# Kernel optimization log

Measured on AMD Instinct MI355X. Metric: run time of the kernel, lower is better.

Reference implementation:

```python
import jax, jax.numpy as jnp
import numpy as np
from jax.ops import segment_sum


def gcn_conv(x, src, dst, W, b, num_nodes):
    # PyG GCNConv: x' = D^{-1/2} (A + I) D^{-1/2} (x @ W) + b
    loops = jnp.arange(num_nodes, dtype=src.dtype)
    s = jnp.concatenate([src, loops])  # source of each edge (incl. self-loops)
    d = jnp.concatenate([dst, loops])  # destination of each edge
    ones = jnp.ones(s.shape[0], dtype=x.dtype)
    deg = segment_sum(ones, d, num_segments=num_nodes)  # in-degree incl. self-loop
    dinv = jnp.where(deg > 0, jax.lax.rsqrt(deg), 0.0)
    norm = dinv[s] * dinv[d]  # [E+N]
    h = x @ W  # [N, C_out] dense transform first (C_out <= C_in typical)
    msg = h[s] * norm[:, None]  # gather + scale  [E+N, C_out]
    out = segment_sum(msg, d, num_segments=num_nodes)  # scatter-add
    return out + b


def setup_inputs() -> dict:
    key = jax.random.key(0)
    k1, k2, k3, k4 = jax.random.split(key, 4)
    N, E = 100000, 1600000
    C_in, C_out = 64, 32
    C_hid = 2 * C_out
    x = jax.random.normal(k1, (N, C_in), dtype=jnp.float32)
    edge_index = jax.random.randint(k2, (2, E), 0, N, dtype=jnp.int64)
    # Glorot-style init for the linear weights, zero bias (PyG defaults)
    W1 = jax.random.normal(k3, (C_in, C_hid), dtype=jnp.float32) * (1.0 / np.sqrt(C_in))
    b1 = jnp.zeros((C_hid,), dtype=jnp.float32)
    W2 = jax.random.normal(k4, (C_hid, C_out), dtype=jnp.float32) * (1.0 / np.sqrt(C_hid))
    b2 = jnp.zeros((C_out,), dtype=jnp.float32)
    return {"x": x, "edge_index": edge_index, "num_nodes": N,
            "W1": W1, "b1": b1, "W2": W2, "b2": b2}


def reference(x, edge_index, num_nodes, W1, b1, W2, b2):
    src, dst = edge_index[0], edge_index[1]
    h = gcn_conv(x, src, dst, W1, b1, num_nodes)
    h = jax.nn.relu(h)
    out = gcn_conv(h, src, dst, W2, b2, num_nodes)
    return out
```

## Files before the change

kernel.cpp:

```cpp
#include <hip/hip_runtime.h>


constexpr int CAP = 4096;
constexpr int NBMAX = 1024;
constexpr int SBCAP = 40960;
constexpr int NSBMAX = 64;
constexpr float QS = 2048.f;
constexpr float QSI = 1.f / 2048.f;

__device__ inline int sxlo(unsigned u) { return (int)(short)(u & 0xffffu); }
__device__ inline int sxhi(unsigned u) { return ((int)u) >> 16; }

__global__ __launch_bounds__(256) void p1a(const int* __restrict__ src,
                                           const int* __restrict__ dst,
                                           int* __restrict__ sbCursor,
                                           unsigned* __restrict__ stg1, int E, int NSB) {
    __shared__ int cnt[NSBMAX];
    __shared__ int cur[NSBMAX];
    int tid = threadIdx.x;
    if (tid < NSBMAX) cnt[tid] = 0;
    __syncthreads();
    int e0 = blockIdx.x * 2048;
    unsigned dv[8];
#pragma unroll
    for (int k = 0; k < 8; ++k) {
        int e = e0 + k * 256 + tid;
        dv[k] = 0u;
        if (e < E) {
            dv[k] = (unsigned)dst[e];
            atomicAdd(&cnt[dv[k] >> 11], 1);
        }
    }
    __syncthreads();
    if (tid < NSB) {
        int c = cnt[tid];
        cur[tid] = c ? atomicAdd(&sbCursor[tid], c) : 0;
    }
    __syncthreads();
#pragma unroll
    for (int k = 0; k < 8; ++k) {
        int e = e0 + k * 256 + tid;
        if (e < E) {
            unsigned d = dv[k];
            int b = d >> 11;
            int slot = atomicAdd(&cur[b], 1);
            if (slot < SBCAP)
                stg1[(size_t)b * SBCAP + slot] = ((unsigned)src[e] << 11) | (d & 2047u);
        }
    }
}

__global__ __launch_bounds__(256) void p1b(const unsigned* __restrict__ stg1,
                                           const int* __restrict__ sbCursor,
                                           int* __restrict__ bucketCursor,
                                           unsigned* __restrict__ staging) {
    __shared__ int cnt[16];
    __shared__ int cur[16];
    int b = blockIdx.x >> 4;
    int s = blockIdx.x & 15;
    int tid = threadIdx.x;
    if (tid < 16) cnt[tid] = 0;
    __syncthreads();
    int sz = sbCursor[b];
    if (sz > SBCAP) sz = SBCAP;
    int lo = (sz * s) >> 4, hi = (sz * (s + 1)) >> 4;
    const unsigned* st = stg1 + (size_t)b * SBCAP;
    for (int i = lo + tid; i < hi; i += 256) atomicAdd(&cnt[(st[i] >> 7) & 15u], 1);
    __syncthreads();
    if (tid < 16) {
        int c = cnt[tid];
        cur[tid] = c ? atomicAdd(&bucketCursor[b * 16 + tid], c) : 0;
    }
    __syncthreads();
    for (int i = lo + tid; i < hi; i += 256) {
        unsigned w = st[i];
        int f = (w >> 7) & 15u;
        int slot = atomicAdd(&cur[f], 1);
        if (slot < CAP)
            staging[(size_t)(b * 16 + f) * CAP + slot] = ((w >> 11) << 7) | (w & 127u);
    }
}

__global__ __launch_bounds__(256) void gemm1(const float* __restrict__ X,
                                             const float* __restrict__ W,
                                             const unsigned* __restrict__ staging,
                                             const int* __restrict__ bucketCursor,
                                             float* __restrict__ dinv,
                                             unsigned short* __restrict__ Hout, int N) {
    constexpr int XS = 65;
    __shared__ float Xs[128 * XS];
    __shared__ float Ws[64 * 64];
    __shared__ int degs[128];
    int tid = threadIdx.x;
    int b = blockIdx.x;
    int rowBase = b * 128;
    if (tid < 128) degs[tid] = 0;
    __syncthreads();
    {
        int size = bucketCursor[b];
        if (size > CAP) size = CAP;
        const unsigned* st = staging + (size_t)b * CAP;
        for (int i = tid; i < size; i += 256) atomicAdd(&degs[st[i] & 127u], 1);
    }
    const float4* Wv = (const float4*)W;
    float4* Wsv = (float4*)Ws;
    for (int i = tid; i < 64 * 64 / 4; i += 256) Wsv[i] = Wv[i];
    const float4* Xv = (const float4*)X;
    for (int v = tid; v < 128 * 16; v += 256) {
        int r = v >> 4, j = v & 15;
        int gr = rowBase + r;
        float4 t = make_float4(0.f, 0.f, 0.f, 0.f);
        if (gr < N) t = Xv[(size_t)gr * 16 + j];
        int bb = r * XS + j * 4;
        Xs[bb] = t.x;
        Xs[bb + 1] = t.y;
        Xs[bb + 2] = t.z;
        Xs[bb + 3] = t.w;
    }
    __syncthreads();
    if (tid < 128) {
        int gn = rowBase + tid;
        if (gn < N) dinv[gn] = rsqrtf((float)(degs[tid] + 1));
    }
    int cg = tid % 8, rg = tid / 8;
    int c0 = cg * 8, r0 = rg * 4;
    float acc[4][8];
#pragma unroll
    for (int i = 0; i < 4; ++i)
#pragma unroll
        for (int j = 0; j < 8; ++j) acc[i][j] = 0.f;
#pragma unroll 8
    for (int k = 0; k < 64; ++k) {
        float4 w0 = *(const float4*)&Ws[k * 64 + c0];
        float4 w1 = *(const float4*)&Ws[k * 64 + c0 + 4];
        float xr[4];
#pragma unroll
        for (int i = 0; i < 4; ++i) xr[i] = Xs[(r0 + i) * XS + k];
#pragma unroll
        for (int i = 0; i < 4; ++i) {
            acc[i][0] = fmaf(xr[i], w0.x, acc[i][0]);
            acc[i][1] = fmaf(xr[i], w0.y, acc[i][1]);
            acc[i][2] = fmaf(xr[i], w0.z, acc[i][2]);
            acc[i][3] = fmaf(xr[i], w0.w, acc[i][3]);
            acc[i][4] = fmaf(xr[i], w1.x, acc[i][4]);
            acc[i][5] = fmaf(xr[i], w1.y, acc[i][5]);
            acc[i][6] = fmaf(xr[i], w1.z, acc[i][6]);
            acc[i][7] = fmaf(xr[i], w1.w, acc[i][7]);
        }
    }
#pragma unroll
    for (int i = 0; i < 4; ++i) {
        int row = rowBase + r0 + i;
        if (row >= N) continue;
        float dq = rsqrtf((float)(degs[r0 + i] + 1)) * QS;
        unsigned short* rp = Hout + (size_t)row * 64 + cg;
#pragma unroll
        for (int j = 0; j < 8; ++j) {
            rp[8 * j] = (unsigned short)(short)(int)(acc[i][j] * dq);
        }
    }
}

__global__ __launch_bounds__(256) void agg1_gemm2(
    const uint4* __restrict__ hs1, const unsigned* __restrict__ staging,
    const int* __restrict__ bucketCursor, const float* __restrict__ dinv,
    const float* __restrict__ b1, const float* __restrict__ W2,
    unsigned short* __restrict__ h2, int N) {
    constexpr int S1 = 65;
    __shared__ int acc[128 * S1];
    __shared__ float Ws[64 * 32];
    __shared__ float b1s[64];
    __shared__ float dns[128];
    int b = blockIdx.x, tid = threadIdx.x;
    int gbase = b * 128;
    const float4* Wv = (const float4*)W2;
    float4* Wsv = (float4*)Ws;
    for (int i = tid; i < 64 * 32 / 4; i += 256) Wsv[i] = Wv[i];
    if (tid < 64) b1s[tid] = QS * b1[tid];
    if (tid < 128) {
        int gn = gbase + tid;
        dns[tid] = (gn < N) ? dinv[gn] : 0.f;
    }
    for (int v = tid; v < 128 * 8; v += 256) {
        int n = v >> 3, j = v & 7;
        int s0 = 0, s1 = 0, s2 = 0, s3 = 0, s4 = 0, s5 = 0, s6 = 0, s7 = 0;
        if (gbase + n < N) {
            uint4 u = hs1[(size_t)(gbase + n) * 8 + j];
            s0 = sxlo(u.x); s1 = sxhi(u.x);
            s2 = sxlo(u.y); s3 = sxhi(u.y);
            s4 = sxlo(u.z); s5 = sxhi(u.z);
            s6 = sxlo(u.w); s7 = sxhi(u.w);
        }
        int* dp = &acc[n * S1 + j];
        dp[0] = s0;  dp[8] = s1;  dp[16] = s2; dp[24] = s3;
        dp[32] = s4; dp[40] = s5; dp[48] = s6; dp[56] = s7;
    }
    __syncthreads();
    int size = bucketCursor[b];
    if (size > CAP) size = CAP;
    const unsigned* st = staging + (size_t)b * CAP;
    int g = tid >> 3, q = tid & 7;
#define ADD8(NN, U)                          \
    {                                        \
        int* ap = &acc[(int)(NN) * S1 + q];  \
        atomicAdd(ap + 0,  sxlo((U).x));     \
        atomicAdd(ap + 8,  sxhi((U).x));     \
        atomicAdd(ap + 16, sxlo((U).y));     \
        atomicAdd(ap + 24, sxhi((U).y));     \
        atomicAdd(ap + 32, sxlo((U).z));     \
        atomicAdd(ap + 40, sxhi((U).z));     \
        atomicAdd(ap + 48, sxlo((U).w));     \
        atomicAdd(ap + 56, sxhi((U).w));     \
    }
    int i = g;
    for (; i + 480 < size; i += 512) {
        unsigned w[16];
        uint4 u[16];
#pragma unroll
        for (int k = 0; k < 16; ++k) w[k] = st[i + 32 * k];
#pragma unroll
        for (int k = 0; k < 16; ++k) u[k] = hs1[(size_t)(w[k] >> 7) * 8 + q];
#pragma unroll
        for (int k = 0; k < 16; ++k) ADD8(w[k] & 127u, u[k])
    }
    for (; i + 224 < size; i += 256) {
        unsigned w[8];
        uint4 u[8];
#pragma unroll
        for (int k = 0; k < 8; ++k) w[k] = st[i + 32 * k];
#pragma unroll
        for (int k = 0; k < 8; ++k) u[k] = hs1[(size_t)(w[k] >> 7) * 8 + q];
#pragma unroll
        for (int k = 0; k < 8; ++k) ADD8(w[k] & 127u, u[k])
    }
    for (; i < size; i += 32) {
        unsigned w = st[i];
        uint4 u = hs1[(size_t)(w >> 7) * 8 + q];
        ADD8(w & 127u, u)
    }
#undef ADD8
    __syncthreads();
    float* af = (float*)acc;
    for (int v = tid; v < 128 * 64; v += 256) {
        int n = v >> 6, c = v & 63;
        af[n * S1 + c] = fmaxf(fmaf((float)acc[n * S1 + c], dns[n], b1s[c]), 0.f);
    }
    __syncthreads();
    int cg = tid & 3, rg = tid >> 2;
    int c0 = cg * 8, r0 = rg * 2;
    float a2[2][8];
#pragma unroll
    for (int i2 = 0; i2 < 2; ++i2)
#pragma unroll
        for (int j = 0; j < 8; ++j) a2[i2][j] = 0.f;
#pragma unroll 8
    for (int k = 0; k < 64; ++k) {
        float4 w0 = *(const float4*)&Ws[k * 32 + c0];
        float4 w1 = *(const float4*)&Ws[k * 32 + c0 + 4];
        float x0 = af[r0 * S1 + k];
        float x1 = af[(r0 + 1) * S1 + k];
        a2[0][0] = fmaf(x0, w0.x, a2[0][0]);
        a2[0][1] = fmaf(x0, w0.y, a2[0][1]);
        a2[0][2] = fmaf(x0, w0.z, a2[0][2]);
        a2[0][3] = fmaf(x0, w0.w, a2[0][3]);
        a2[0][4] = fmaf(x0, w1.x, a2[0][4]);
        a2[0][5] = fmaf(x0, w1.y, a2[0][5]);
        a2[0][6] = fmaf(x0, w1.z, a2[0][6]);
        a2[0][7] = fmaf(x0, w1.w, a2[0][7]);
        a2[1][0] = fmaf(x1, w0.x, a2[1][0]);
        a2[1][1] = fmaf(x1, w0.y, a2[1][1]);
        a2[1][2] = fmaf(x1, w0.z, a2[1][2]);
        a2[1][3] = fmaf(x1, w0.w, a2[1][3]);
        a2[1][4] = fmaf(x1, w1.x, a2[1][4]);
        a2[1][5] = fmaf(x1, w1.y, a2[1][5]);
        a2[1][6] = fmaf(x1, w1.z, a2[1][6]);
        a2[1][7] = fmaf(x1, w1.w, a2[1][7]);
    }
#pragma unroll
    for (int i2 = 0; i2 < 2; ++i2) {
        int row = gbase + r0 + i2;
        if (row >= N) continue;
        float dn = dns[r0 + i2];
        unsigned short* rp = h2 + (size_t)row * 32;
#pragma unroll
        for (int j = 0; j < 8; ++j) {
            rp[8 * (j & 3) + 2 * cg + (j >> 2)] =
                (unsigned short)(short)(int)(a2[i2][j] * dn);
        }
    }
}

__global__ __launch_bounds__(256) void agg2(const uint4* __restrict__ hs2,
                                            const unsigned* __restrict__ staging,
                                            const int* __restrict__ bucketCursor,
                                            const float* __restrict__ dinv,
                                            const float* __restrict__ b2,
                                            float* __restrict__ out, int N) {
    constexpr int S2 = 33;
    __shared__ int acc[128 * S2];
    __shared__ float b2s[32];
    int b = blockIdx.x, tid = threadIdx.x;
    int gbase = b * 128;
    if (tid < 32) b2s[tid] = b2[tid];
    for (int v = tid; v < 128 * 4; v += 256) {
        int n = v >> 2, j = v & 3;
        int s0 = 0, s1 = 0, s2 = 0, s3 = 0, s4 = 0, s5 = 0, s6 = 0, s7 = 0;
        if (gbase + n < N) {
            uint4 u = hs2[(size_t)(gbase + n) * 4 + j];
            s0 = sxlo(u.x); s1 = sxhi(u.x);
            s2 = sxlo(u.y); s3 = sxhi(u.y);
            s4 = sxlo(u.z); s5 = sxhi(u.z);
            s6 = sxlo(u.w); s7 = sxhi(u.w);
        }
        int* dp = &acc[n * S2 + j];
        dp[0] = s0;  dp[4] = s1;  dp[8] = s2;  dp[12] = s3;
        dp[16] = s4; dp[20] = s5; dp[24] = s6; dp[28] = s7;
    }
    __syncthreads();
    int size = bucketCursor[b];
    if (size > CAP) size = CAP;
    const unsigned* st = staging + (size_t)b * CAP;
    int g = tid >> 2, q = tid & 3;
#define ADD8(NN, U)                          \
    {                                        \
        int* ap = &acc[(int)(NN) * S2 + q];  \
        atomicAdd(ap + 0,  sxlo((U).x));     \
        atomicAdd(ap + 4,  sxhi((U).x));     \
        atomicAdd(ap + 8,  sxlo((U).y));     \
        atomicAdd(ap + 12, sxhi((U).y));     \
        atomicAdd(ap + 16, sxlo((U).z));     \
        atomicAdd(ap + 20, sxhi((U).z));     \
        atomicAdd(ap + 24, sxlo((U).w));     \
        atomicAdd(ap + 28, sxhi((U).w));     \
    }
    int i = g;
    for (; i + 960 < size; i += 1024) {
        unsigned w[16];
        uint4 u[16];
#pragma unroll
        for (int k = 0; k < 16; ++k) w[k] = st[i + 64 * k];
#pragma unroll
        for (int k = 0; k < 16; ++k) u[k] = hs2[(size_t)(w[k] >> 7) * 4 + q];
#pragma unroll
        for (int k = 0; k < 16; ++k) ADD8(w[k] & 127u, u[k])
    }
    for (; i + 448 < size; i += 512) {
        unsigned w[8];
        uint4 u[8];
#pragma unroll
        for (int k = 0; k < 8; ++k) w[k] = st[i + 64 * k];
#pragma unroll
        for (int k = 0; k < 8; ++k) u[k] = hs2[(size_t)(w[k] >> 7) * 4 + q];
#pragma unroll
        for (int k = 0; k < 8; ++k) ADD8(w[k] & 127u, u[k])
    }
    for (; i < size; i += 64) {
        unsigned w = st[i];
        uint4 u = hs2[(size_t)(w >> 7) * 4 + q];
        ADD8(w & 127u, u)
    }
#undef ADD8
    __syncthreads();
    for (int v = tid; v < 128 * 32; v += 256) {
        int n = v >> 5, c = v & 31;
        int gn = gbase + n;
        if (gn >= N) continue;
        out[(size_t)gn * 32 + c] = fmaf((float)acc[n * S2 + c], dinv[gn] * QSI, b2s[c]);
    }
}

extern "C" void kernel_launch(void* const* d_in, const int* in_sizes, int n_in,
                              void* d_out, int out_size, void* d_ws, size_t ws_size,
                              hipStream_t stream) {
    const float* x = (const float*)d_in[0];
    const int* ei = (const int*)d_in[1];
    const float* W1 = (const float*)d_in[3];
    const float* b1 = (const float*)d_in[4];
    const float* W2 = (const float*)d_in[5];
    const float* b2 = (const float*)d_in[6];

    constexpr int CIN = 64, CHID = 64, COUT = 32;
    const int N = in_sizes[0] / CIN;
    const int E = in_sizes[1] / 2;
    const int* src = ei;
    const int* dst = ei + E;
    const int NSB = (N + 2047) >> 11;

    char* p = (char*)d_ws;
    auto carve = [&](size_t bytes) -> void* {
        void* q = (void*)p;
        p += (bytes + 255) & ~(size_t)255;
        return q;
    };
    int* sbCursor = (int*)carve((size_t)NSBMAX * 4);
    int* bucketCursor = (int*)carve((size_t)NBMAX * 4);
    float* dinv = (float*)carve((size_t)N * 4);
    unsigned* stg1 = (unsigned*)carve((size_t)NSB * SBCAP * 4);
    unsigned* staging = (unsigned*)carve((size_t)NSB * 16 * CAP * 4);
    unsigned* h1 = (unsigned*)carve((size_t)N * CHID * 2);
    unsigned* h2 = stg1;

    size_t zbytes = (size_t)((char*)(bucketCursor + NBMAX) - (char*)sbCursor);
    hipMemsetAsync(sbCursor, 0, zbytes, stream);
    p1a<<<(E + 2047) / 2048, 256, 0, stream>>>(src, dst, sbCursor, stg1, E, NSB);
    p1b<<<NSB * 16, 256, 0, stream>>>(stg1, sbCursor, bucketCursor, staging);
    gemm1<<<(N + 127) / 128, 256, 0, stream>>>(x, W1, staging, bucketCursor, dinv,
                                               (unsigned short*)h1, N);
    agg1_gemm2<<<NSB * 16, 256, 0, stream>>>((const uint4*)h1, staging, bucketCursor, dinv,
                                             b1, W2, (unsigned short*)h2, N);
    agg2<<<NSB * 16, 256, 0, stream>>>((const uint4*)h2, staging, bucketCursor, dinv, b2,
                                       (float*)d_out, N);
}
```

Measured before the change: 217.0 us.

## Halve destination bucket size to 64 nodes for aggregation kernels

Destination buckets shrink from 128 to 64 nodes, giving 32 buckets per superblock instead of 16. This doubles the block count for the two aggregation kernels and halves their shared-memory accumulators, aiming for more occupancy and parallelism on the scatter-add phase. gemm1 still handles 128 rows by reading two buckets, and the second GEMM now computes one row per thread. Per-block fixed overhead doubles, and smaller buckets with a 2048 capacity leave less headroom for skewed in-degrees.

```diff
diff --git a/kernel.cpp b/kernel.cpp
--- a/kernel.cpp
+++ b/kernel.cpp
@@ -1,8 +1,8 @@
 #include <hip/hip_runtime.h>
 
 
-constexpr int CAP = 4096;
-constexpr int NBMAX = 1024;
+constexpr int CAP = 2048;
+constexpr int NBMAX = 2048;
 constexpr int SBCAP = 40960;
 constexpr int NSBMAX = 64;
 constexpr float QS = 2048.f;
@@ -54,30 +54,30 @@
                                            const int* __restrict__ sbCursor,
                                            int* __restrict__ bucketCursor,
                                            unsigned* __restrict__ staging) {
-    __shared__ int cnt[16];
-    __shared__ int cur[16];
+    __shared__ int cnt[32];
+    __shared__ int cur[32];
     int b = blockIdx.x >> 4;
     int s = blockIdx.x & 15;
     int tid = threadIdx.x;
-    if (tid < 16) cnt[tid] = 0;
+    if (tid < 32) cnt[tid] = 0;
     __syncthreads();
     int sz = sbCursor[b];
     if (sz > SBCAP) sz = SBCAP;
     int lo = (sz * s) >> 4, hi = (sz * (s + 1)) >> 4;
     const unsigned* st = stg1 + (size_t)b * SBCAP;
-    for (int i = lo + tid; i < hi; i += 256) atomicAdd(&cnt[(st[i] >> 7) & 15u], 1);
-    __syncthreads();
-    if (tid < 16) {
+    for (int i = lo + tid; i < hi; i += 256) atomicAdd(&cnt[(st[i] >> 6) & 31u], 1);
+    __syncthreads();
+    if (tid < 32) {
         int c = cnt[tid];
-        cur[tid] = c ? atomicAdd(&bucketCursor[b * 16 + tid], c) : 0;
+        cur[tid] = c ? atomicAdd(&bucketCursor[b * 32 + tid], c) : 0;
     }
     __syncthreads();
     for (int i = lo + tid; i < hi; i += 256) {
         unsigned w = st[i];
-        int f = (w >> 7) & 15u;
+        int f = (w >> 6) & 31u;
         int slot = atomicAdd(&cur[f], 1);
         if (slot < CAP)
-            staging[(size_t)(b * 16 + f) * CAP + slot] = ((w >> 11) << 7) | (w & 127u);
+            staging[(size_t)(b * 32 + f) * CAP + slot] = ((w >> 11) << 6) | (w & 63u);
     }
 }
 
@@ -97,10 +97,14 @@
     if (tid < 128) degs[tid] = 0;
     __syncthreads();
     {
-        int size = bucketCursor[b];
-        if (size > CAP) size = CAP;
-        const unsigned* st = staging + (size_t)b * CAP;
-        for (int i = tid; i < size; i += 256) atomicAdd(&degs[st[i] & 127u], 1);
+        int sz0 = bucketCursor[2 * b];
+        if (sz0 > CAP) sz0 = CAP;
+        const unsigned* st0 = staging + (size_t)(2 * b) * CAP;
+        for (int i = tid; i < sz0; i += 256) atomicAdd(&degs[st0[i] & 63u], 1);
+        int sz1 = bucketCursor[2 * b + 1];
+        if (sz1 > CAP) sz1 = CAP;
+        const unsigned* st1 = staging + (size_t)(2 * b + 1) * CAP;
+        for (int i = tid; i < sz1; i += 256) atomicAdd(&degs[64 + (st1[i] & 63u)], 1);
     }
     const float4* Wv = (const float4*)W;
     float4* Wsv = (float4*)Ws;
@@ -167,21 +171,21 @@
     const float* __restrict__ b1, const float* __restrict__ W2,
     unsigned short* __restrict__ h2, int N) {
     constexpr int S1 = 65;
-    __shared__ int acc[128 * S1];
+    __shared__ int acc[64 * S1];
     __shared__ float Ws[64 * 32];
     __shared__ float b1s[64];
-    __shared__ float dns[128];
+    __shared__ float dns[64];
     int b = blockIdx.x, tid = threadIdx.x;
-    int gbase = b * 128;
+    int gbase = b * 64;
     const float4* Wv = (const float4*)W2;
     float4* Wsv = (float4*)Ws;
     for (int i = tid; i < 64 * 32 / 4; i += 256) Wsv[i] = Wv[i];
     if (tid < 64) b1s[tid] = QS * b1[tid];
-    if (tid < 128) {
-        int gn = gbase + tid;
-        dns[tid] = (gn < N) ? dinv[gn] : 0.f;
-    }
-    for (int v = tid; v < 128 * 8; v += 256) {
+    if (tid >= 64 && tid < 128) {
+        int gn = gbase + tid - 64;
+        dns[tid - 64] = (gn < N) ? dinv[gn] : 0.f;
+    }
+    for (int v = tid; v < 64 * 8; v += 256) {
         int n = v >> 3, j = v & 7;
         int s0 = 0, s1 = 0, s2 = 0, s3 = 0, s4 = 0, s5 = 0, s6 = 0, s7 = 0;
         if (gbase + n < N) {
@@ -219,9 +223,9 @@
 #pragma unroll
         for (int k = 0; k < 16; ++k) w[k] = st[i + 32 * k];
 #pragma unroll
-        for (int k = 0; k < 16; ++k) u[k] = hs1[(size_t)(w[k] >> 7) * 8 + q];
-#pragma unroll
-        for (int k = 0; k < 16; ++k) ADD8(w[k] & 127u, u[k])
+        for (int k = 0; k < 16; ++k) u[k] = hs1[(size_t)(w[k] >> 6) * 8 + q];
+#pragma unroll
+        for (int k = 0; k < 16; ++k) ADD8(w[k] & 63u, u[k])
     }
     for (; i + 224 < size; i += 256) {
         unsigned w[8];
@@ -229,63 +233,49 @@
 #pragma unroll
         for (int k = 0; k < 8; ++k) w[k] = st[i + 32 * k];
 #pragma unroll
-        for (int k = 0; k < 8; ++k) u[k] = hs1[(size_t)(w[k] >> 7) * 8 + q];
-#pragma unroll
-        for (int k = 0; k < 8; ++k) ADD8(w[k] & 127u, u[k])
+        for (int k = 0; k < 8; ++k) u[k] = hs1[(size_t)(w[k] >> 6) * 8 + q];
+#pragma unroll
+        for (int k = 0; k < 8; ++k) ADD8(w[k] & 63u, u[k])
     }
     for (; i < size; i += 32) {
         unsigned w = st[i];
-        uint4 u = hs1[(size_t)(w >> 7) * 8 + q];
-        ADD8(w & 127u, u)
+        uint4 u = hs1[(size_t)(w >> 6) * 8 + q];
+        ADD8(w & 63u, u)
     }
 #undef ADD8
     __syncthreads();
     float* af = (float*)acc;
-    for (int v = tid; v < 128 * 64; v += 256) {
+    for (int v = tid; v < 64 * 64; v += 256) {
         int n = v >> 6, c = v & 63;
         af[n * S1 + c] = fmaxf(fmaf((float)acc[n * S1 + c], dns[n], b1s[c]), 0.f);
     }
     __syncthreads();
     int cg = tid & 3, rg = tid >> 2;
-    int c0 = cg * 8, r0 = rg * 2;
-    float a2[2][8];
-#pragma unroll
-    for (int i2 = 0; i2 < 2; ++i2)
-#pragma unroll
-        for (int j = 0; j < 8; ++j) a2[i2][j] = 0.f;
+    int c0 = cg * 8;
+    float a2[8];
+#pragma unroll
+    for (int j = 0; j < 8; ++j) a2[j] = 0.f;
 #pragma unroll 8
     for (int k = 0; k < 64; ++k) {
         float4 w0 = *(const float4*)&Ws[k * 32 + c0];
         float4 w1 = *(const float4*)&Ws[k * 32 + c0 + 4];
-        float x0 = af[r0 * S1 + k];
-        float x1 = af[(r0 + 1) * S1 + k];
-        a2[0][0] = fmaf(x0, w0.x, a2[0][0]);
-        a2[0][1] = fmaf(x0, w0.y, a2[0][1]);
-        a2[0][2] = fmaf(x0, w0.z, a2[0][2]);
-        a2[0][3] = fmaf(x0, w0.w, a2[0][3]);
-        a2[0][4] = fmaf(x0, w1.x, a2[0][4]);
-        a2[0][5] = fmaf(x0, w1.y, a2[0][5]);
-        a2[0][6] = fmaf(x0, w1.z, a2[0][6]);
-        a2[0][7] = fmaf(x0, w1.w, a2[0][7]);
-        a2[1][0] = fmaf(x1, w0.x, a2[1][0]);
-        a2[1][1] = fmaf(x1, w0.y, a2[1][1]);
-        a2[1][2] = fmaf(x1, w0.z, a2[1][2]);
-        a2[1][3] = fmaf(x1, w0.w, a2[1][3]);
-        a2[1][4] = fmaf(x1, w1.x, a2[1][4]);
-        a2[1][5] = fmaf(x1, w1.y, a2[1][5]);
-        a2[1][6] = fmaf(x1, w1.z, a2[1][6]);
-        a2[1][7] = fmaf(x1, w1.w, a2[1][7]);
-    }
-#pragma unroll
-    for (int i2 = 0; i2 < 2; ++i2) {
-        int row = gbase + r0 + i2;
-        if (row >= N) continue;
-        float dn = dns[r0 + i2];
+        float x0 = af[rg * S1 + k];
+        a2[0] = fmaf(x0, w0.x, a2[0]);
+        a2[1] = fmaf(x0, w0.y, a2[1]);
+        a2[2] = fmaf(x0, w0.z, a2[2]);
+        a2[3] = fmaf(x0, w0.w, a2[3]);
+        a2[4] = fmaf(x0, w1.x, a2[4]);
+        a2[5] = fmaf(x0, w1.y, a2[5]);
+        a2[6] = fmaf(x0, w1.z, a2[6]);
+        a2[7] = fmaf(x0, w1.w, a2[7]);
+    }
+    int row = gbase + rg;
+    if (row < N) {
+        float dn = dns[rg];
         unsigned short* rp = h2 + (size_t)row * 32;
 #pragma unroll
         for (int j = 0; j < 8; ++j) {
-            rp[8 * (j & 3) + 2 * cg + (j >> 2)] =
-                (unsigned short)(short)(int)(a2[i2][j] * dn);
+            rp[8 * (j & 3) + 2 * cg + (j >> 2)] = (unsigned short)(short)(int)(a2[j] * dn);
         }
     }
 }
@@ -297,12 +287,12 @@
                                             const float* __restrict__ b2,
                                             float* __restrict__ out, int N) {
     constexpr int S2 = 33;
-    __shared__ int acc[128 * S2];
+    __shared__ int acc[64 * S2];
     __shared__ float b2s[32];
     int b = blockIdx.x, tid = threadIdx.x;
-    int gbase = b * 128;
+    int gbase = b * 64;
     if (tid < 32) b2s[tid] = b2[tid];
-    for (int v = tid; v < 128 * 4; v += 256) {
+    for (int v = tid; v < 64 * 4; v += 256) {
         int n = v >> 2, j = v & 3;
         int s0 = 0, s1 = 0, s2 = 0, s3 = 0, s4 = 0, s5 = 0, s6 = 0, s7 = 0;
         if (gbase + n < N) {
@@ -334,34 +324,24 @@
         atomicAdd(ap + 28, sxhi((U).w));     \
     }
     int i = g;
-    for (; i + 960 < size; i += 1024) {
-        unsigned w[16];
-        uint4 u[16];
-#pragma unroll
-        for (int k = 0; k < 16; ++k) w[k] = st[i + 64 * k];
-#pragma unroll
-        for (int k = 0; k < 16; ++k) u[k] = hs2[(size_t)(w[k] >> 7) * 4 + q];
-#pragma unroll
-        for (int k = 0; k < 16; ++k) ADD8(w[k] & 127u, u[k])
-    }
     for (; i + 448 < size; i += 512) {
         unsigned w[8];
         uint4 u[8];
 #pragma unroll
         for (int k = 0; k < 8; ++k) w[k] = st[i + 64 * k];
 #pragma unroll
-        for (int k = 0; k < 8; ++k) u[k] = hs2[(size_t)(w[k] >> 7) * 4 + q];
-#pragma unroll
-        for (int k = 0; k < 8; ++k) ADD8(w[k] & 127u, u[k])
+        for (int k = 0; k < 8; ++k) u[k] = hs2[(size_t)(w[k] >> 6) * 4 + q];
+#pragma unroll
+        for (int k = 0; k < 8; ++k) ADD8(w[k] & 63u, u[k])
     }
     for (; i < size; i += 64) {
         unsigned w = st[i];
-        uint4 u = hs2[(size_t)(w >> 7) * 4 + q];
-        ADD8(w & 127u, u)
+        uint4 u = hs2[(size_t)(w >> 6) * 4 + q];
+        ADD8(w & 63u, u)
     }
 #undef ADD8
     __syncthreads();
-    for (int v = tid; v < 128 * 32; v += 256) {
+    for (int v = tid; v < 64 * 32; v += 256) {
         int n = v >> 5, c = v & 31;
         int gn = gbase + n;
         if (gn >= N) continue;
@@ -385,6 +365,7 @@
     const int* src = ei;
     const int* dst = ei + E;
     const int NSB = (N + 2047) >> 11;
+    const int NBT = NSB * 32;
 
     char* p = (char*)d_ws;
     auto carve = [&](size_t bytes) -> void* {
@@ -396,7 +377,7 @@
     int* bucketCursor = (int*)carve((size_t)NBMAX * 4);
     float* dinv = (float*)carve((size_t)N * 4);
     unsigned* stg1 = (unsigned*)carve((size_t)NSB * SBCAP * 4);
-    unsigned* staging = (unsigned*)carve((size_t)NSB * 16 * CAP * 4);
+    unsigned* staging = (unsigned*)carve((size_t)NBT * CAP * 4);
     unsigned* h1 = (unsigned*)carve((size_t)N * CHID * 2);
     unsigned* h2 = stg1;
 
@@ -406,8 +387,8 @@
     p1b<<<NSB * 16, 256, 0, stream>>>(stg1, sbCursor, bucketCursor, staging);
     gemm1<<<(N + 127) / 128, 256, 0, stream>>>(x, W1, staging, bucketCursor, dinv,
                                                (unsigned short*)h1, N);
-    agg1_gemm2<<<NSB * 16, 256, 0, stream>>>((const uint4*)h1, staging, bucketCursor, dinv,
-                                             b1, W2, (unsigned short*)h2, N);
-    agg2<<<NSB * 16, 256, 0, stream>>>((const uint4*)h2, staging, bucketCursor, dinv, b2,
-                                       (float*)d_out, N);
-}
+    agg1_gemm2<<<NBT, 256, 0, stream>>>((const uint4*)h1, staging, bucketCursor, dinv,
+                                        b1, W2, (unsigned short*)h2, N);
+    agg2<<<NBT, 256, 0, stream>>>((const uint4*)h2, staging, bucketCursor, dinv, b2,
+                                  (float*)d_out, N);
+}
```

New measurement: 209.2 us. 1.04x faster.
